# Kernel optimization log

Measured on AMD Instinct MI355X. Metric: run time of the kernel, lower is better.

## Reference

```python
import jax, jax.numpy as jnp
import numpy as np

N = 100_000   # nodes
E = 1_600_000 # edges
G = 2_000     # graphs
P = 4_096     # ranking pairs
F_IN = 9      # num_node_features
U = 128       # model_units


def _linear_init(key, fan_in, fan_out):
    k1, k2 = jax.random.split(key)
    s = 1.0 / np.sqrt(fan_in)
    W = jax.random.uniform(k1, (fan_in, fan_out), jnp.float32, -s, s)
    b = jax.random.uniform(k2, (fan_out,), jnp.float32, -s, s)
    return W, b


def setup_inputs() -> dict:
    key = jax.random.key(0)
    ks = jax.random.split(key, 12)
    x = jax.random.normal(ks[0], (N, F_IN), jnp.float32)
    edge_index = jax.random.randint(ks[1], (2, E), 0, N, dtype=jnp.int32)
    # sorted, even node->graph assignment; every graph non-empty
    batch = (jnp.arange(N, dtype=jnp.int32) * G) // N
    idx_a = jax.random.randint(ks[2], (P,), 0, G, dtype=jnp.int32)
    idx_b = jax.random.randint(ks[3], (P,), 0, G, dtype=jnp.int32)
    W_in, b_in = _linear_init(ks[4], F_IN, U)
    W1, b1 = _linear_init(ks[5], U, U)
    W2, b2 = _linear_init(ks[6], U, U)
    Wf1, bf1 = _linear_init(ks[7], U, U)
    Wf2, bf2 = _linear_init(ks[8], U, 32)
    Wf3, bf3 = _linear_init(ks[9], 32, 1)
    return dict(x=x, edge_index=edge_index, batch=batch, idx_a=idx_a, idx_b=idx_b,
                W_in=W_in, b_in=b_in, W1=W1, b1=b1, W2=W2, b2=b2,
                Wf1=Wf1, bf1=bf1, Wf2=Wf2, bf2=bf2, Wf3=Wf3, bf3=bf3)


def reference(x, edge_index, batch, idx_a, idx_b,
              W_in, b_in, W1, b1, W2, b2, Wf1, bf1, Wf2, bf2, Wf3, bf3):
    src, dst = edge_index[0], edge_index[1]
    n = x.shape[0]
    # GCN symmetric norm with self-loops: deg counts in-edges + self-loop
    deg = jax.ops.segment_sum(jnp.ones(src.shape[0], jnp.float32), dst, num_segments=n) + 1.0
    dinv = jax.lax.rsqrt(deg)
    edge_norm = (dinv[src] * dinv[dst])[:, None]   # [E,1]
    self_norm = (dinv * dinv)[:, None]             # [N,1]

    def gcn(h, W, b):
        h = h @ W
        agg = jax.ops.segment_sum(h[src] * edge_norm, dst, num_segments=n)
        return agg + h * self_norm + b

    h = jnp.tanh(gcn(x, W_in, b_in))
    # dropout with training=False is identity
    h = jnp.tanh(gcn(h, W1, b1))
    h = jnp.tanh(gcn(h, W2, b2))
    h = jnp.tanh(h @ Wf1 + bf1)
    h = jnp.tanh(h @ Wf2 + bf2)
    h = h @ Wf3 + bf3  # [N,1]

    # global_mean_pool over graphs
    counts = jax.ops.segment_sum(jnp.ones(n, jnp.float32), batch, num_segments=G)
    util = jax.ops.segment_sum(h, batch, num_segments=G) / jnp.maximum(counts, 1.0)[:, None]  # [G,1]

    u = util[:, 0]
    out = jax.nn.sigmoid(u[idx_b] - u[idx_a])  # [P]
    return out, util
```

## Files before the change

### kernel.cpp

```cpp
#include <hip/hip_runtime.h>
#include <hip/hip_bf16.h>
#include <math.h>


#define U 128
#define LDA 136
#define WB 9
#define WSZ 512
#define NJ1 256

typedef __attribute__((ext_vector_type(8))) short bf16x8;
typedef __attribute__((ext_vector_type(4))) float f32x4;

__device__ __forceinline__ unsigned short f2bf(float f) {
    unsigned u = __float_as_uint(f);
    unsigned r = (u + 0x7fffu + ((u >> 16) & 1u)) >> 16;
    return (unsigned short)r;
}
__device__ __forceinline__ float bf_lo(unsigned u) { return __uint_as_float(u << 16); }
__device__ __forceinline__ float bf_hi(unsigned u) { return __uint_as_float(u & 0xffff0000u); }

__global__ __launch_bounds__(256) void k_hist1(const int* __restrict__ dst,
                                               int* __restrict__ hist_g, int E, int nw) {
    __shared__ int h[256];
    int b = blockIdx.x;
    for (int i = threadIdx.x; i < nw; i += 256) h[i] = 0;
    __syncthreads();
    int ch = (E + NJ1 - 1) / NJ1;
    int e0 = b * ch, e1 = min(e0 + ch, E);
    for (int e = e0 + threadIdx.x; e < e1; e += 256)
        atomicAdd(&h[dst[e] >> WB], 1);
    __syncthreads();
    for (int w = threadIdx.x; w < nw; w += 256) hist_g[w * NJ1 + b] = h[w];
}

__global__ __launch_bounds__(256) void k_escan1(int* __restrict__ a,
                                                int* __restrict__ bsum, int n) {
    __shared__ int sc[256];
    int t = threadIdx.x, b = blockIdx.x;
    int base = b * 1024 + t * 4;
    int v[4];
    int s = 0;
    #pragma unroll
    for (int j = 0; j < 4; ++j) {
        int idx = base + j;
        int d = (idx < n) ? a[idx] : 0;
        v[j] = s;
        s += d;
    }
    sc[t] = s;
    __syncthreads();
    for (int off = 1; off < 256; off <<= 1) {
        int x = (t >= off) ? sc[t - off] : 0;
        __syncthreads();
        sc[t] += x;
        __syncthreads();
    }
    int excl = sc[t] - s;
    #pragma unroll
    for (int j = 0; j < 4; ++j) {
        int idx = base + j;
        if (idx < n) a[idx] = v[j] + excl;
    }
    if (t == 255) bsum[b] = sc[255];
}

__global__ __launch_bounds__(256) void k_escan2(int* __restrict__ a,
                                                const int* __restrict__ bsum,
                                                int nb, int n) {
    __shared__ int sc[256];
    int t = threadIdx.x;
    int v = (t < nb) ? bsum[t] : 0;
    sc[t] = v;
    __syncthreads();
    for (int off = 1; off < 256; off <<= 1) {
        int u = (t >= off) ? sc[t - off] : 0;
        __syncthreads();
        sc[t] += u;
        __syncthreads();
    }
    int myoff = (blockIdx.x > 0) ? (sc[blockIdx.x] - bsum[blockIdx.x]) : 0;
    int base = blockIdx.x * 1024;
    #pragma unroll
    for (int j = 0; j < 4; ++j) {
        int idx = base + t + j * 256;
        if (idx < n) a[idx] += myoff;
    }
}

__global__ __launch_bounds__(256) void k_bucket(const int* __restrict__ src,
                                                const int* __restrict__ dst,
                                                const int* __restrict__ hist_g,
                                                int2* __restrict__ eb, int E, int nw) {
    __shared__ int lcur[256];
    int b = blockIdx.x;
    for (int w = threadIdx.x; w < nw; w += 256) lcur[w] = hist_g[w * NJ1 + b];
    __syncthreads();
    int ch = (E + NJ1 - 1) / NJ1;
    int e0 = b * ch, e1 = min(e0 + ch, E);
    for (int e = e0 + threadIdx.x; e < e1; e += 256) {
        int d = dst[e];
        int pos = atomicAdd(&lcur[d >> WB], 1);
        eb[pos] = make_int2(src[e], d);
    }
}

__global__ __launch_bounds__(256) void k_deg2(const int2* __restrict__ eb,
                                              const int* __restrict__ hist_g,
                                              int* __restrict__ deg, int E, int nw, int N) {
    __shared__ int h[WSZ];
    int w = blockIdx.x;
    h[threadIdx.x] = 0;
    h[threadIdx.x + 256] = 0;
    __syncthreads();
    int s0 = hist_g[w * NJ1];
    int s1 = (w + 1 < nw) ? hist_g[(w + 1) * NJ1] : E;
    for (int i = s0 + threadIdx.x; i < s1; i += 256)
        atomicAdd(&h[eb[i].y & (WSZ - 1)], 1);
    __syncthreads();
    int base = w << WB;
    if (base + threadIdx.x < N) deg[base + threadIdx.x] = h[threadIdx.x];
    if (base + 256 + threadIdx.x < N) deg[base + 256 + threadIdx.x] = h[256 + threadIdx.x];
}

__global__ __launch_bounds__(256) void k_scan1(const int* __restrict__ deg,
                                               int* __restrict__ rowptr1,
                                               int* __restrict__ bsum, int N) {
    __shared__ int sc[256];
    int t = threadIdx.x, b = blockIdx.x;
    int base = b * 1024 + t * 4;
    int v[4];
    int s = 0;
    #pragma unroll
    for (int j = 0; j < 4; ++j) {
        int idx = base + j;
        int d = (idx < N) ? deg[idx] : 0;
        s += d;
        v[j] = s;
    }
    sc[t] = s;
    __syncthreads();
    for (int off = 1; off < 256; off <<= 1) {
        int x = (t >= off) ? sc[t - off] : 0;
        __syncthreads();
        sc[t] += x;
        __syncthreads();
    }
    int excl = sc[t] - s;
    #pragma unroll
    for (int j = 0; j < 4; ++j) {
        int idx = base + j;
        if (idx < N) rowptr1[idx] = v[j] + excl;
    }
    if (t == 255) bsum[b] = sc[255];
}

__global__ __launch_bounds__(256) void k_scan23(int* __restrict__ rowptr,
                                                const int* __restrict__ bsum,
                                                int nb, int N) {
    __shared__ int sc[256];
    __shared__ int bo[256];
    int t = threadIdx.x;
    int v = (t < nb) ? bsum[t] : 0;
    sc[t] = v;
    __syncthreads();
    for (int off = 1; off < 256; off <<= 1) {
        int u = (t >= off) ? sc[t - off] : 0;
        __syncthreads();
        sc[t] += u;
        __syncthreads();
    }
    bo[t] = sc[t] - v;
    __syncthreads();
    int i = blockIdx.x * 256 + t;
    if (i < N) rowptr[1 + i] += bo[i >> 10];
    if (i == 0) rowptr[0] = 0;
}

__global__ __launch_bounds__(256) void k_scatter2(const int2* __restrict__ eb,
                                                  const int* __restrict__ hist_g,
                                                  const int* __restrict__ rowptr,
                                                  int* __restrict__ csr_src,
                                                  int E, int nw, int N) {
    __shared__ int cur[WSZ];
    int w = blockIdx.x;
    int base = w << WB;
    int i0 = base + threadIdx.x, i1 = base + 256 + threadIdx.x;
    cur[threadIdx.x] = (i0 < N) ? rowptr[i0] : 0;
    cur[threadIdx.x + 256] = (i1 < N) ? rowptr[i1] : 0;
    __syncthreads();
    int s0 = hist_g[w * NJ1];
    int s1 = (w + 1 < nw) ? hist_g[(w + 1) * NJ1] : E;
    for (int i = s0 + threadIdx.x; i < s1; i += 256) {
        int2 e = eb[i];
        int pos = atomicAdd(&cur[e.y & (WSZ - 1)], 1);
        csr_src[pos] = e.x;
    }
}

__global__ __launch_bounds__(256) void k_prep(const int* __restrict__ deg,
                                              const float* __restrict__ x,
                                              const int* __restrict__ batch,
                                              const float* __restrict__ W1,
                                              const float* __restrict__ W2,
                                              const float* __restrict__ Wf1,
                                              const float* __restrict__ Wf2,
                                              float* __restrict__ dinv,
                                              float* __restrict__ xs,
                                              int* __restrict__ cnt,
                                              unsigned short* __restrict__ W1t,
                                              unsigned short* __restrict__ W2t,
                                              unsigned short* __restrict__ Wf1t,
                                              unsigned short* __restrict__ Wf2t, int N) {
    int t = blockIdx.x * 256 + threadIdx.x;
    if (t < N) {
        float dv = rsqrtf((float)deg[t] + 1.0f);
        dinv[t] = dv;
        #pragma unroll
        for (int k = 0; k < 9; ++k) xs[t * 9 + k] = x[t * 9 + k] * dv;
        atomicAdd(&cnt[batch[t]], 1);
    }
    if (t < 16384) {
        int n = t >> 7, k = t & 127;
        W1t[n * 128 + k] = f2bf(W1[k * 128 + n]);
        Wf1t[n * 128 + k] = f2bf(Wf1[k * 128 + n]);
    } else if (t < 32768) {
        int i = t - 16384, n = i >> 7, k = i & 127;
        W2t[n * 128 + k] = f2bf(W2[k * 128 + n]);
    } else if (t < 36864) {
        int i = t - 32768, n = i >> 7, k = i & 127;
        Wf2t[n * 128 + k] = f2bf(Wf2[k * 32 + n]);
    }
}

__global__ __launch_bounds__(256) void k_aggx(const float* __restrict__ xs,
                                              const int* __restrict__ rowptr,
                                              const int* __restrict__ csr_src,
                                              const float* __restrict__ dinv,
                                              float* __restrict__ xa, int N) {
    int node = blockIdx.x * 16 + (threadIdx.x >> 4);
    if (node >= N) return;
    int lane = threadIdx.x & 15;
    bool act = lane < 9;
    int s = rowptr[node], e = rowptr[node + 1];
    float a0 = 0.0f, a1 = 0.0f, a2 = 0.0f, a3 = 0.0f;
    int i = s;
    for (; i + 4 <= e; i += 4) {
        int s0 = csr_src[i], s1 = csr_src[i + 1];
        int s2 = csr_src[i + 2], s3 = csr_src[i + 3];
        if (act) {
            a0 += xs[s0 * 9 + lane];
            a1 += xs[s1 * 9 + lane];
            a2 += xs[s2 * 9 + lane];
            a3 += xs[s3 * 9 + lane];
        }
    }
    for (; i < e; ++i) {
        int s0 = csr_src[i];
        if (act) a0 += xs[s0 * 9 + lane];
    }
    if (act) {
        float dv = dinv[node];
        xa[node * 9 + lane] = dv * (a0 + a1 + a2 + a3 + xs[node * 9 + lane]);
    }
}

__global__ void k_gemm_in9(const float* __restrict__ xa, const float* __restrict__ Wi,
                           const float* __restrict__ bi, unsigned short* __restrict__ T,
                           int N) {
    int t = blockIdx.x * 256 + threadIdx.x;
    if (t < N * U) {
        int n = t >> 7, c = t & 127;
        const float* xr = xa + n * 9;
        float acc = bi[c];
        #pragma unroll
        for (int k = 0; k < 9; ++k) acc += xr[k] * Wi[k * U + c];
        T[t] = f2bf(tanhf(acc));
    }
}

__global__ __launch_bounds__(256) void k_gemm_mfma(const unsigned short* __restrict__ A,
                                                   const unsigned short* __restrict__ Wt,
                                                   const float* __restrict__ dinv,
                                                   unsigned short* __restrict__ Out, int N) {
    const int tid = threadIdx.x;
    const int wave = tid >> 6, lane = tid & 63;
    const int m16 = lane & 15, q = lane >> 4;
    const int row0 = blockIdx.x * 64 + wave * 16;
    int arow_idx = row0 + m16;
    if (arow_idx >= N) arow_idx = N - 1;
    const bf16x8* arow = (const bf16x8*)(A + (size_t)arow_idx * U + q * 8);
    f32x4 acc[8];
    #pragma unroll
    for (int t = 0; t < 8; ++t) acc[t] = (f32x4){0.f, 0.f, 0.f, 0.f};
    #pragma unroll
    for (int kc = 0; kc < 4; ++kc) {
        bf16x8 af = arow[kc * 4];
        #pragma unroll
        for (int t = 0; t < 8; ++t) {
            bf16x8 bfr = *(const bf16x8*)(Wt + ((t * 16 + m16) * 128 + kc * 32 + q * 8));
            acc[t] = __builtin_amdgcn_mfma_f32_16x16x32_bf16(af, bfr, acc[t], 0, 0, 0);
        }
    }
    float dv[4];
    #pragma unroll
    for (int r = 0; r < 4; ++r) {
        int gr = row0 + q * 4 + r;
        dv[r] = (gr < N) ? dinv[gr] : 0.0f;
    }
    #pragma unroll
    for (int t = 0; t < 8; ++t) {
        #pragma unroll
        for (int r = 0; r < 4; ++r) {
            int gr = row0 + q * 4 + r;
            if (gr < N) Out[(size_t)gr * U + t * 16 + m16] = f2bf(acc[t][r] * dv[r]);
        }
    }
}

__global__ __launch_bounds__(256) void k_aggb(const unsigned short* __restrict__ Tb,
                                              const int* __restrict__ rowptr,
                                              const int* __restrict__ csr_src,
                                              const float* __restrict__ dinv,
                                              const float* __restrict__ bias,
                                              unsigned short* __restrict__ Out, int N) {
    int node = blockIdx.x * 4 + (threadIdx.x >> 6);
    if (node >= N) return;
    int lane = threadIdx.x & 63;
    const unsigned* T32 = (const unsigned*)Tb;
    float ax = 0.0f, ay = 0.0f, bx = 0.0f, by = 0.0f;
    int s = rowptr[node], e = rowptr[node + 1];
    int i = s;
    for (; i + 8 <= e; i += 8) {
        int idx[8];
        #pragma unroll
        for (int u = 0; u < 8; ++u) idx[u] = csr_src[i + u];
        unsigned uv[8];
        #pragma unroll
        for (int u = 0; u < 8; ++u) uv[u] = T32[idx[u] * 64 + lane];
        #pragma unroll
        for (int u = 0; u < 8; u += 2) {
            ax += bf_lo(uv[u]) + bf_lo(uv[u + 1]);
            ay += bf_hi(uv[u]) + bf_hi(uv[u + 1]);
        }
    }
    for (; i + 4 <= e; i += 4) {
        int s0 = csr_src[i], s1 = csr_src[i + 1];
        int s2 = csr_src[i + 2], s3 = csr_src[i + 3];
        unsigned u0 = T32[s0 * 64 + lane];
        unsigned u1 = T32[s1 * 64 + lane];
        unsigned u2 = T32[s2 * 64 + lane];
        unsigned u3 = T32[s3 * 64 + lane];
        ax += bf_lo(u0) + bf_lo(u1);
        ay += bf_hi(u0) + bf_hi(u1);
        bx += bf_lo(u2) + bf_lo(u3);
        by += bf_hi(u2) + bf_hi(u3);
    }
    for (; i < e; ++i) {
        int s0 = csr_src[i];
        unsigned u0 = T32[s0 * 64 + lane];
        ax += bf_lo(u0);
        ay += bf_hi(u0);
    }
    float dv = dinv[node];
    unsigned su = T32[node * 64 + lane];
    float2 bb = *(const float2*)&bias[lane * 2];
    float ox = tanhf(dv * (ax + bx + bf_lo(su)) + bb.x);
    float oy = tanhf(dv * (ay + by + bf_hi(su)) + bb.y);
    unsigned o = (unsigned)f2bf(ox) | ((unsigned)f2bf(oy) << 16);
    ((unsigned*)Out)[node * 64 + lane] = o;
}

__global__ __launch_bounds__(256) void k_mlp(const unsigned short* __restrict__ H,
                                             const unsigned short* __restrict__ Wf1t,
                                             const float* __restrict__ bf1,
                                             const unsigned short* __restrict__ Wf2t,
                                             const float* __restrict__ bf2,
                                             const float* __restrict__ Wf3,
                                             const float* __restrict__ bf3,
                                             const int* __restrict__ batch,
                                             float* __restrict__ util_sum, int N) {
    __shared__ unsigned short H2[64 * LDA];
    const int tid = threadIdx.x;
    const int wave = tid >> 6, lane = tid & 63;
    const int m16 = lane & 15, q = lane >> 4;
    const int row0 = blockIdx.x * 64 + wave * 16;
    int arow_idx = row0 + m16;
    if (arow_idx >= N) arow_idx = N - 1;
    const bf16x8* arow = (const bf16x8*)(H + (size_t)arow_idx * U + q * 8);
    f32x4 acc[8];
    #pragma unroll
    for (int t = 0; t < 8; ++t) acc[t] = (f32x4){0.f, 0.f, 0.f, 0.f};
    #pragma unroll
    for (int kc = 0; kc < 4; ++kc) {
        bf16x8 af = arow[kc * 4];
        #pragma unroll
        for (int t = 0; t < 8; ++t) {
            bf16x8 bfr = *(const bf16x8*)(Wf1t + ((t * 16 + m16) * 128 + kc * 32 + q * 8));
            acc[t] = __builtin_amdgcn_mfma_f32_16x16x32_bf16(af, bfr, acc[t], 0, 0, 0);
        }
    }
    #pragma unroll
    for (int t = 0; t < 8; ++t) {
        float b = bf1[t * 16 + m16];
        #pragma unroll
        for (int r = 0; r < 4; ++r) {
            int lr = wave * 16 + q * 4 + r;
            H2[lr * LDA + t * 16 + m16] = f2bf(tanhf(acc[t][r] + b));
        }
    }
    f32x4 acc2[2];
    acc2[0] = (f32x4){0.f, 0.f, 0.f, 0.f};
    acc2[1] = (f32x4){0.f, 0.f, 0.f, 0.f};
    const unsigned short* h2row = &H2[(wave * 16 + m16) * LDA + q * 8];
    #pragma unroll
    for (int kc = 0; kc < 4; ++kc) {
        bf16x8 af = *(const bf16x8*)(h2row + kc * 32);
        #pragma unroll
        for (int t = 0; t < 2; ++t) {
            bf16x8 bfr = *(const bf16x8*)(Wf2t + ((t * 16 + m16) * 128 + kc * 32 + q * 8));
            acc2[t] = __builtin_amdgcn_mfma_f32_16x16x32_bf16(af, bfr, acc2[t], 0, 0, 0);
        }
    }
    float b2lo = bf2[m16], b2hi = bf2[m16 + 16];
    float w3lo = Wf3[m16], w3hi = Wf3[m16 + 16];
    float bf3v = bf3[0];
    #pragma unroll
    for (int r = 0; r < 4; ++r) {
        float t0 = tanhf(acc2[0][r] + b2lo);
        float t1 = tanhf(acc2[1][r] + b2hi);
        float v = t0 * w3lo + t1 * w3hi;
        v += __shfl_xor(v, 1);
        v += __shfl_xor(v, 2);
        v += __shfl_xor(v, 4);
        v += __shfl_xor(v, 8);
        if (m16 == 0) {
            int n = row0 + q * 4 + r;
            if (n < N) atomicAdd(&util_sum[batch[n]], v + bf3v);
        }
    }
}

__global__ void k_out(const float* __restrict__ us, const int* __restrict__ cnt,
                      const int* __restrict__ ia, const int* __restrict__ ib,
                      float* __restrict__ out, int P, int G) {
    int t = blockIdx.x * 256 + threadIdx.x;
    if (t < G) out[P + t] = us[t] / fmaxf((float)cnt[t], 1.0f);
    if (t < P) {
        int a = ia[t], b = ib[t];
        float ua = us[a] / fmaxf((float)cnt[a], 1.0f);
        float ub = us[b] / fmaxf((float)cnt[b], 1.0f);
        out[t] = 1.0f / (1.0f + expf(-(ub - ua)));
    }
}

extern "C" void kernel_launch(void* const* d_in, const int* in_sizes, int n_in,
                              void* d_out, int out_size, void* d_ws, size_t ws_size,
                              hipStream_t stream) {
    const float* x     = (const float*)d_in[0];
    const int*   eidx  = (const int*)d_in[1];
    const int*   batch = (const int*)d_in[2];
    const int*   idx_a = (const int*)d_in[3];
    const int*   idx_b = (const int*)d_in[4];
    const float* W_in  = (const float*)d_in[5];
    const float* b_in  = (const float*)d_in[6];
    const float* W1    = (const float*)d_in[7];
    const float* b1    = (const float*)d_in[8];
    const float* W2    = (const float*)d_in[9];
    const float* b2    = (const float*)d_in[10];
    const float* Wf1   = (const float*)d_in[11];
    const float* bf1   = (const float*)d_in[12];
    const float* Wf2   = (const float*)d_in[13];
    const float* bf2   = (const float*)d_in[14];
    const float* Wf3   = (const float*)d_in[15];
    const float* bf3   = (const float*)d_in[16];
    float* out = (float*)d_out;

    const int N = in_sizes[0] / 9;
    const int E = in_sizes[1] / 2;
    const int P = in_sizes[3];
    const int G = out_size - P;

    const int* src = eidx;
    const int* dst = eidx + E;

    const int nw = (N + WSZ - 1) >> WB;
    const int nb = (N + 1023) / 1024;
    const int nh = nw * NJ1;
    const int nbh = (nh + 1023) / 1024;

    char* ws = (char*)d_ws;
    size_t off = 0;
    auto take = [&](size_t bytes) -> void* {
        void* p = ws + off;
        off = (off + bytes + 255) & ~(size_t)255;
        return p;
    };
    int*   deg      = (int*)  take((size_t)N * 4);
    float* dinv     = (float*)take((size_t)N * 4);
    int*   rowptr   = (int*)  take((size_t)(N + 1) * 4);
    int*   bsum     = (int*)  take(256 * 4);
    int*   bsum2    = (int*)  take(256 * 4);
    int*   hist_g   = (int*)  take((size_t)nh * 4);
    int2*  eb       = (int2*) take((size_t)E * 8);
    int*   csr_src  = (int*)  take((size_t)E * 4);
    float* xs       = (float*)take((size_t)N * 9 * 4);
    float* xa       = (float*)take((size_t)N * 9 * 4);
    unsigned short* bufA = (unsigned short*)take((size_t)N * U * 2);
    unsigned short* Tb   = (unsigned short*)take((size_t)N * U * 2);
    unsigned short* W1t  = (unsigned short*)take(128 * 128 * 2);
    unsigned short* W2t  = (unsigned short*)take(128 * 128 * 2);
    unsigned short* Wf1t = (unsigned short*)take(128 * 128 * 2);
    unsigned short* Wf2t = (unsigned short*)take(32 * 128 * 2);
    float* util_sum = (float*)take((size_t)G * 4 + (size_t)G * 4);
    int*   cnt      = (int*)(util_sum + G);
    (void)ws_size;

    hipMemsetAsync(util_sum, 0, (size_t)G * 8, stream);

    k_hist1<<<NJ1, 256, 0, stream>>>(dst, hist_g, E, nw);
    k_escan1<<<nbh, 256, 0, stream>>>(hist_g, bsum2, nh);
    k_escan2<<<nbh, 256, 0, stream>>>(hist_g, bsum2, nbh, nh);
    k_bucket<<<NJ1, 256, 0, stream>>>(src, dst, hist_g, eb, E, nw);
    k_deg2<<<nw, 256, 0, stream>>>(eb, hist_g, deg, E, nw, N);
    k_prep<<<(N + 255) / 256, 256, 0, stream>>>(deg, x, batch, W1, W2, Wf1, Wf2,
                                                dinv, xs, cnt, W1t, W2t, Wf1t, Wf2t, N);
    k_scan1<<<nb, 256, 0, stream>>>(deg, rowptr + 1, bsum, N);
    k_scan23<<<(N + 255) / 256, 256, 0, stream>>>(rowptr, bsum, nb, N);
    k_scatter2<<<nw, 256, 0, stream>>>(eb, hist_g, rowptr, csr_src, E, nw, N);

    const int aggGrid  = (N + 3) / 4;
    const int gemmGrid = (N + 63) / 64;

    k_aggx<<<(N + 15) / 16, 256, 0, stream>>>(xs, rowptr, csr_src, dinv, xa, N);
    k_gemm_in9<<<((size_t)N * U + 255) / 256, 256, 0, stream>>>(xa, W_in, b_in, bufA, N);

    k_gemm_mfma<<<gemmGrid, 256, 0, stream>>>(bufA, W1t, dinv, Tb, N);
    k_aggb<<<aggGrid, 256, 0, stream>>>(Tb, rowptr, csr_src, dinv, b1, bufA, N);
    k_gemm_mfma<<<gemmGrid, 256, 0, stream>>>(bufA, W2t, dinv, Tb, N);
    k_aggb<<<aggGrid, 256, 0, stream>>>(Tb, rowptr, csr_src, dinv, b2, bufA, N);

    k_mlp<<<gemmGrid, 256, 0, stream>>>(bufA, Wf1t, bf1, Wf2t, bf2, Wf3, bf3,
                                        batch, util_sum, N);

    int mx = (P > G ? P : G);
    k_out<<<(mx + 255) / 256, 256, 0, stream>>>(util_sum, cnt, idx_a, idx_b, out, P, G);
}
```

Baseline: 519.9 us.

## Keep MLP weights in registers across tiles and pre-reduce graph sums in LDS

The MLP head kernel now has each wave handle four 16-row tiles. Wf1/Wf2 fragments are loaded into registers once per wave and reused across those tiles, and the next tile's activations are prefetched while the current one computes. Per-row global atomics into util_sum are replaced by LDS atomics into a small per-block graph-sum array, which is then flushed with a few global atomics. This cuts redundant weight loads and global atomic traffic, at the cost of much higher register pressure. The LDS reduction also assumes a 256-node block spans at most 8 graphs, which holds only for the sorted, evenly spread batch.

Result: faster. 476.8 us (-8.3%).

```diff
diff --git a/kernel.cpp b/kernel.cpp
--- a/kernel.cpp
+++ b/kernel.cpp
@@ -371,72 +371,112 @@
     ((unsigned*)Out)[node * 64 + lane] = o;
 }
 
-__global__ __launch_bounds__(256) void k_mlp(const unsigned short* __restrict__ H,
-                                             const unsigned short* __restrict__ Wf1t,
-                                             const float* __restrict__ bf1,
-                                             const unsigned short* __restrict__ Wf2t,
-                                             const float* __restrict__ bf2,
-                                             const float* __restrict__ Wf3,
-                                             const float* __restrict__ bf3,
-                                             const int* __restrict__ batch,
-                                             float* __restrict__ util_sum, int N) {
-    __shared__ unsigned short H2[64 * LDA];
+__global__ __launch_bounds__(256, 2) void k_mlp(const unsigned short* __restrict__ H,
+                                                const unsigned short* __restrict__ Wf1t,
+                                                const float* __restrict__ bf1,
+                                                const unsigned short* __restrict__ Wf2t,
+                                                const float* __restrict__ bf2,
+                                                const float* __restrict__ Wf3,
+                                                const float* __restrict__ bf3,
+                                                const int* __restrict__ batch,
+                                                float* __restrict__ util_sum,
+                                                int N, int G) {
+    __shared__ unsigned short H2[4][16 * LDA];
+    __shared__ float gsum[8];
     const int tid = threadIdx.x;
+    if (tid < 8) gsum[tid] = 0.0f;
     const int wave = tid >> 6, lane = tid & 63;
     const int m16 = lane & 15, q = lane >> 4;
-    const int row0 = blockIdx.x * 64 + wave * 16;
-    int arow_idx = row0 + m16;
-    if (arow_idx >= N) arow_idx = N - 1;
-    const bf16x8* arow = (const bf16x8*)(H + (size_t)arow_idx * U + q * 8);
-    f32x4 acc[8];
-    #pragma unroll
-    for (int t = 0; t < 8; ++t) acc[t] = (f32x4){0.f, 0.f, 0.f, 0.f};
+    const int blk0 = blockIdx.x * 256;
+    const int g0 = batch[min(blk0, N - 1)];
+    bf16x8 w1[4][8], w2[4][2];
     #pragma unroll
     for (int kc = 0; kc < 4; ++kc) {
-        bf16x8 af = arow[kc * 4];
+        #pragma unroll
+        for (int t = 0; t < 8; ++t)
+            w1[kc][t] = *(const bf16x8*)(Wf1t + ((t * 16 + m16) * 128 + kc * 32 + q * 8));
+        #pragma unroll
+        for (int t = 0; t < 2; ++t)
+            w2[kc][t] = *(const bf16x8*)(Wf2t + ((t * 16 + m16) * 128 + kc * 32 + q * 8));
+    }
+    float b1v[8];
+    #pragma unroll
+    for (int t = 0; t < 8; ++t) b1v[t] = bf1[t * 16 + m16];
+    const float b2lo = bf2[m16], b2hi = bf2[m16 + 16];
+    const float w3lo = Wf3[m16], w3hi = Wf3[m16 + 16];
+    const float bf3v = bf3[0];
+    __syncthreads();
+    unsigned short* h2s = H2[wave];
+    const int wbase = blk0 + wave * 64;
+    bf16x8 a[4];
+    {
+        int ar = wbase + m16;
+        if (ar >= N) ar = N - 1;
+        const bf16x8* arow = (const bf16x8*)(H + (size_t)ar * U + q * 8);
+        #pragma unroll
+        for (int kc = 0; kc < 4; ++kc) a[kc] = arow[kc * 4];
+    }
+    for (int tile = 0; tile < 4; ++tile) {
+        const int row0 = wbase + tile * 16;
+        bf16x8 an[4];
+        if (tile < 3) {
+            int ar = row0 + 16 + m16;
+            if (ar >= N) ar = N - 1;
+            const bf16x8* arow = (const bf16x8*)(H + (size_t)ar * U + q * 8);
+            #pragma unroll
+            for (int kc = 0; kc < 4; ++kc) an[kc] = arow[kc * 4];
+        }
+        f32x4 acc[8];
+        #pragma unroll
+        for (int t = 0; t < 8; ++t) acc[t] = (f32x4){0.f, 0.f, 0.f, 0.f};
+        #pragma unroll
+        for (int kc = 0; kc < 4; ++kc) {
+            #pragma unroll
+            for (int t = 0; t < 8; ++t)
+                acc[t] = __builtin_amdgcn_mfma_f32_16x16x32_bf16(a[kc], w1[kc][t], acc[t], 0, 0, 0);
+        }
         #pragma unroll
         for (int t = 0; t < 8; ++t) {
-            bf16x8 bfr = *(const bf16x8*)(Wf1t + ((t * 16 + m16) * 128 + kc * 32 + q * 8));
-            acc[t] = __builtin_amdgcn_mfma_f32_16x16x32_bf16(af, bfr, acc[t], 0, 0, 0);
-        }
-    }
-    #pragma unroll
-    for (int t = 0; t < 8; ++t) {
-        float b = bf1[t * 16 + m16];
+            #pragma unroll
+            for (int r = 0; r < 4; ++r) {
+                int lr = q * 4 + r;
+                h2s[lr * LDA + t * 16 + m16] = f2bf(tanhf(acc[t][r] + b1v[t]));
+            }
+        }
+        f32x4 acc2[2];
+        acc2[0] = (f32x4){0.f, 0.f, 0.f, 0.f};
+        acc2[1] = (f32x4){0.f, 0.f, 0.f, 0.f};
+        const unsigned short* h2row = h2s + m16 * LDA + q * 8;
+        #pragma unroll
+        for (int kc = 0; kc < 4; ++kc) {
+            bf16x8 af = *(const bf16x8*)(h2row + kc * 32);
+            #pragma unroll
+            for (int t = 0; t < 2; ++t)
+                acc2[t] = __builtin_amdgcn_mfma_f32_16x16x32_bf16(af, w2[kc][t], acc2[t], 0, 0, 0);
+        }
         #pragma unroll
         for (int r = 0; r < 4; ++r) {
-            int lr = wave * 16 + q * 4 + r;
-            H2[lr * LDA + t * 16 + m16] = f2bf(tanhf(acc[t][r] + b));
-        }
-    }
-    f32x4 acc2[2];
-    acc2[0] = (f32x4){0.f, 0.f, 0.f, 0.f};
-    acc2[1] = (f32x4){0.f, 0.f, 0.f, 0.f};
-    const unsigned short* h2row = &H2[(wave * 16 + m16) * LDA + q * 8];
-    #pragma unroll
-    for (int kc = 0; kc < 4; ++kc) {
-        bf16x8 af = *(const bf16x8*)(h2row + kc * 32);
-        #pragma unroll
-        for (int t = 0; t < 2; ++t) {
-            bf16x8 bfr = *(const bf16x8*)(Wf2t + ((t * 16 + m16) * 128 + kc * 32 + q * 8));
-            acc2[t] = __builtin_amdgcn_mfma_f32_16x16x32_bf16(af, bfr, acc2[t], 0, 0, 0);
-        }
-    }
-    float b2lo = bf2[m16], b2hi = bf2[m16 + 16];
-    float w3lo = Wf3[m16], w3hi = Wf3[m16 + 16];
-    float bf3v = bf3[0];
-    #pragma unroll
-    for (int r = 0; r < 4; ++r) {
-        float t0 = tanhf(acc2[0][r] + b2lo);
-        float t1 = tanhf(acc2[1][r] + b2hi);
-        float v = t0 * w3lo + t1 * w3hi;
-        v += __shfl_xor(v, 1);
-        v += __shfl_xor(v, 2);
-        v += __shfl_xor(v, 4);
-        v += __shfl_xor(v, 8);
-        if (m16 == 0) {
-            int n = row0 + q * 4 + r;
-            if (n < N) atomicAdd(&util_sum[batch[n]], v + bf3v);
+            float t0 = tanhf(acc2[0][r] + b2lo);
+            float t1 = tanhf(acc2[1][r] + b2hi);
+            float v = t0 * w3lo + t1 * w3hi;
+            v += __shfl_xor(v, 1);
+            v += __shfl_xor(v, 2);
+            v += __shfl_xor(v, 4);
+            v += __shfl_xor(v, 8);
+            if (m16 == 0) {
+                int n = row0 + q * 4 + r;
+                if (n < N) atomicAdd(&gsum[batch[n] - g0], v + bf3v);
+            }
+        }
+        #pragma unroll
+        for (int kc = 0; kc < 4; ++kc) a[kc] = an[kc];
+    }
+    __syncthreads();
+    if (tid < 8) {
+        int g = g0 + tid;
+        if (g < G) {
+            float s = gsum[tid];
+            if (s != 0.0f) atomicAdd(&util_sum[g], s);
         }
     }
 }
@@ -540,8 +580,8 @@
     k_gemm_mfma<<<gemmGrid, 256, 0, stream>>>(bufA, W2t, dinv, Tb, N);
     k_aggb<<<aggGrid, 256, 0, stream>>>(Tb, rowptr, csr_src, dinv, b2, bufA, N);
 
-    k_mlp<<<gemmGrid, 256, 0, stream>>>(bufA, Wf1t, bf1, Wf2t, bf2, Wf3, bf3,
-                                        batch, util_sum, N);
+    k_mlp<<<(N + 255) / 256, 256, 0, stream>>>(bufA, Wf1t, bf1, Wf2t, bf2, Wf3, bf3,
+                                               batch, util_sum, N, G);
 
     int mx = (P > G ? P : G);
     k_out<<<(mx + 255) / 256, 256, 0, stream>>>(util_sum, cnt, idx_a, idx_b, out, P, G);
```
